# Kernel tuning notes

Hardware: AMD Instinct MI355X
Metric: run time of the kernel (lower is better)

## Reference

```python
import jax, jax.numpy as jnp
import numpy as np

NUM_HEADS = 16

def rotate_half(x):
    h = x.shape[-1] // 2
    return jnp.concatenate([-x[..., h:], x[..., :h]], axis=-1)

def setup_inputs() -> dict:
    key = jax.random.key(0)
    k1, k2, k3 = jax.random.split(key, 3)
    B, S, H = 2, 2048, 1024
    x = jax.random.normal(k1, (B, S, H), dtype=jnp.float32)
    W_qkv = jax.random.normal(k2, (3 * H, H), dtype=jnp.float32) * (1.0 / np.sqrt(H))
    W_proj = jax.random.normal(k3, (H, H), dtype=jnp.float32) * (1.0 / np.sqrt(H))
    return {"x": x, "W_qkv": W_qkv, "W_proj": W_proj}

def reference(x, W_qkv, W_proj):
    B, S, H = x.shape
    nH = NUM_HEADS
    hd = H // nH
    # QKV projection (bias=False): y = x @ W.T
    qkv = jnp.einsum('bsh,oh->bso', x, W_qkv)  # [B,S,3H]
    q, k, v = jnp.split(qkv, 3, axis=-1)
    def to_heads(t):
        return t.reshape(B, S, nH, hd).transpose(0, 2, 1, 3)  # [B,nH,S,hd]
    q, k, v = to_heads(q), to_heads(k), to_heads(v)
    # RoPE on first half of head_dim; freqs dim = hd//2
    half = hd // 2
    inv_freq = 1.0 / (10000.0 ** (jnp.arange(0, hd, 2, dtype=jnp.float32) / hd))  # [hd//2]
    t = jnp.arange(S, dtype=jnp.float32)
    freqs = t[:, None] * inv_freq[None, :]  # [S, hd//2]
    cos = jnp.cos(freqs)[None, None]  # [1,1,S,hd//2]
    sin = jnp.sin(freqs)[None, None]
    q_half, q_rest = q[..., :half], q[..., half:]
    k_half, k_rest = k[..., :half], k[..., half:]
    q_rot = q_half * cos + rotate_half(q_half) * sin
    k_rot = k_half * cos + rotate_half(k_half) * sin
    q = jnp.concatenate([q_rot, q_rest], axis=-1)
    k = jnp.concatenate([k_rot, k_rest], axis=-1)
    # scaled dot-product attention (no mask, dropout=0 / eval)
    scale = 1.0 / np.sqrt(hd)
    att = jnp.einsum('bhqd,bhkd->bhqk', q, k) * scale  # [B,nH,S,S]
    att = jax.nn.softmax(att, axis=-1)
    out = jnp.einsum('bhqk,bhkd->bhqd', att, v)  # [B,nH,S,hd]
    out = out.transpose(0, 2, 1, 3).reshape(B, S, H)
    return jnp.einsum('bsh,oh->bso', out, W_proj)
```

## Files before the change

### kernel.cpp

```cpp
#include <hip/hip_runtime.h>
#include <math.h>

#define SEQ  2048
#define NHD  16
#define HD   64
#define HDIM 1024

typedef short s16x8 __attribute__((ext_vector_type(8)));
typedef short s16x4 __attribute__((ext_vector_type(4)));
typedef float f32x4 __attribute__((ext_vector_type(4)));

typedef const __attribute__((address_space(1))) unsigned int* gp_t;
typedef __attribute__((address_space(3))) unsigned int* lp_t;

__device__ __forceinline__ void async16(const short* g, short* l) {
    __builtin_amdgcn_global_load_lds((gp_t)g, (lp_t)l, 16, 0, 0);
}

__device__ __forceinline__ short f2bf(float f) {
    unsigned int u = __float_as_uint(f);
    u += 0x7fff + ((u >> 16) & 1);
    return (short)(u >> 16);
}
__device__ __forceinline__ float bf2f(short s) {
    return __uint_as_float(((unsigned int)(unsigned short)s) << 16);
}

__global__ void detect_k(const unsigned short* __restrict__ x, int* __restrict__ flag) {
    int cnt = 0;
    #pragma unroll 4
    for (int j = 0; j < 32; ++j) {
        unsigned short h = x[threadIdx.x * 32 + j];
        int e = (h >> 7) & 0xFF;
        cnt += (e >= 100 && e <= 140) ? 1 : 0;
    }
    __shared__ int tot;
    if (threadIdx.x == 0) tot = 0;
    __syncthreads();
    atomicAdd(&tot, cnt);
    __syncthreads();
    if (threadIdx.x == 0) *flag = (tot > (8192 * 9) / 10) ? 1 : 0;
}

#define XG4  (4096 * 1024 / 4)
#define WQG4 (3072 * 1024 / 4)
#define WPG4 (1024 * 1024 / 4)
__global__ void cvt_all_k(const void* __restrict__ xr, const void* __restrict__ wqr,
                          const void* __restrict__ wpr, short* __restrict__ xo,
                          short* __restrict__ wqo, short* __restrict__ wpo,
                          const int* __restrict__ flag) {
    int i = blockIdx.x * 256 + threadIdx.x;
    const void* in; short* out; int j;
    if (i < XG4)             { in = xr;  out = xo;  j = i; }
    else if (i < XG4 + WQG4) { in = wqr; out = wqo; j = i - XG4; }
    else                     { in = wpr; out = wpo; j = i - XG4 - WQG4; }
    if (*flag) {
        ((s16x4*)out)[j] = ((const s16x4*)in)[j];
    } else {
        f32x4 v = ((const f32x4*)in)[j];
        s16x4 r;
        r[0] = f2bf(v[0]); r[1] = f2bf(v[1]);
        r[2] = f2bf(v[2]); r[3] = f2bf(v[3]);
        ((s16x4*)out)[j] = r;
    }
}

__global__ void rope_tab_k(float2* __restrict__ tab) {
    int i = blockIdx.x * 256 + threadIdx.x;
    if (i >= SEQ * 32) return;
    int s = i >> 5, d = i & 31;
    float invf = (float)pow(10000.0, -(double)d / 32.0);
    float af = (float)s * invf;
    double a = (double)af;
    tab[i] = make_float2((float)cos(a), (float)sin(a));
}

template<int MODE>
__global__ __launch_bounds__(256, 2)
void gemm_bt(const short* __restrict__ A, const short* __restrict__ B,
             short* __restrict__ q, short* __restrict__ kbuf, short* __restrict__ vt,
             float* __restrict__ C, const float2* __restrict__ tab,
             int K, int N) {
    __shared__ __align__(16) short As[2][128 * 32];
    __shared__ __align__(16) short Bs[2][128 * 32];
    const int tid  = threadIdx.x;
    const int w    = tid >> 6, lane = tid & 63;
    const int quad = lane >> 4, l16 = lane & 15;
    const int wm = (w >> 1) * 64, wn = (w & 1) * 64;
    const int rowA0 = blockIdx.y * 128;
    const int colB0 = blockIdx.x * 128;

    auto stage = [&](int buf, int kb) {
        #pragma unroll
        for (int i = 0; i < 2; ++i) {
            int cidx = i * 256 + w * 64 + lane;
            int row = cidx >> 2, sc = cidx & 3;
            int c = sc ^ (row & 3);
            async16(&A[(long)(rowA0 + row) * K + kb + c * 8],
                    &As[buf][(i * 256 + w * 64) * 8]);
            async16(&B[(long)(colB0 + row) * K + kb + c * 8],
                    &Bs[buf][(i * 256 + w * 64) * 8]);
        }
    };

    f32x4 acc[4][4] = {};
    stage(0, 0);

    for (int kb = 0, it = 0; kb < K; kb += 32, ++it) {
        const int cur = it & 1;
        __syncthreads();
        if (kb + 32 < K) stage(cur ^ 1, kb + 32);

        s16x8 af[4], bfr[4];
        const int slot = quad ^ (l16 & 3);
        #pragma unroll
        for (int mi = 0; mi < 4; ++mi)
            af[mi] = *(const s16x8*)&As[cur][(wm + mi * 16 + l16) * 32 + slot * 8];
        #pragma unroll
        for (int ni = 0; ni < 4; ++ni)
            bfr[ni] = *(const s16x8*)&Bs[cur][(wn + ni * 16 + l16) * 32 + slot * 8];
        #pragma unroll
        for (int mi = 0; mi < 4; ++mi)
            #pragma unroll
            for (int ni = 0; ni < 4; ++ni)
                acc[mi][ni] = __builtin_amdgcn_mfma_f32_16x16x32_bf16(
                    af[mi], bfr[ni], acc[mi][ni], 0, 0, 0);
    }

    const int cb = colB0 + wn;
    if (MODE == 1) {
        #pragma unroll
        for (int mi = 0; mi < 4; ++mi) {
            #pragma unroll
            for (int r = 0; r < 4; ++r) {
                int gm = rowA0 + wm + mi * 16 + quad * 4 + r;
                float* cp = C + (long)gm * N + cb + l16;
                #pragma unroll
                for (int ni = 0; ni < 4; ++ni)
                    cp[ni * 16] = acc[mi][ni][r];
            }
        }
        return;
    }
    const int sector = cb >> 10;
    const int head   = (cb & 1023) >> 6;
    if (sector < 2) {
        const float sc = (sector == 0) ? 0.18033688f : 1.0f;
        __syncthreads();
        short* arena = (w < 2) ? (&As[0][0] + w * 2048) : (&Bs[0][0] + (w - 2) * 2048);
        const int gmb = rowA0 + wm;
        const int b = gmb >> 11, s0 = gmb & 2047;
        short* dst0 = (sector == 0 ? q : kbuf)
                    + ((long)((b * NHD + head) * SEQ + s0)) * HD;
        #pragma unroll
        for (int hh = 0; hh < 2; ++hh) {
            #pragma unroll
            for (int m2 = 0; m2 < 2; ++m2) {
                int mi = hh * 2 + m2;
                #pragma unroll
                for (int r = 0; r < 4; ++r) {
                    int lrow = m2 * 16 + quad * 4 + r;
                    int s = s0 + hh * 32 + lrow;
                    float v0 = acc[mi][0][r], v1 = acc[mi][1][r];
                    float v2 = acc[mi][2][r], v3 = acc[mi][3][r];
                    float2 cs0 = tab[s * 32 + l16];
                    float2 cs1 = tab[s * 32 + 16 + l16];
                    float n0 = v0 * cs0.x - v1 * cs0.y;
                    float n1 = v1 * cs1.x + v0 * cs1.y;
                    arena[lrow * 64 + l16]      = f2bf(n0 * sc);
                    arena[lrow * 64 + l16 + 16] = f2bf(n1 * sc);
                    arena[lrow * 64 + l16 + 32] = f2bf(v2 * sc);
                    arena[lrow * 64 + l16 + 48] = f2bf(v3 * sc);
                }
            }
            #pragma unroll
            for (int it = 0; it < 4; ++it) {
                int chunk = it * 64 + lane;
                int row = chunk >> 3, cc = chunk & 7;
                s16x8 vv = *(const s16x8*)&arena[row * 64 + cc * 8];
                *(s16x8*)&dst0[(hh * 32 + row) * HD + cc * 8] = vv;
            }
        }
    } else {
        #pragma unroll
        for (int mi = 0; mi < 4; ++mi) {
            int srow = rowA0 + wm + mi * 16 + quad * 4;
            int b = srow >> 11, s0 = srow & 2047;
            #pragma unroll
            for (int ni = 0; ni < 4; ++ni) {
                s16x4 pk;
                #pragma unroll
                for (int r = 0; r < 4; ++r) pk[r] = f2bf(acc[mi][ni][r]);
                *(s16x4*)&vt[((long)((b * NHD + head) * HD + ni * 16 + l16)) * SEQ + s0] = pk;
            }
        }
    }
}

__global__ __launch_bounds__(256, 4)
void flash_attn(const short* __restrict__ Q, const short* __restrict__ K,
                const short* __restrict__ Vt, short* __restrict__ opart,
                float* __restrict__ lpart, int nt) {
    __shared__ __align__(16) short Ks[2][64 * 64];
    __shared__ __align__(16) short Vs[2][64 * 64];
    const int tid  = threadIdx.x;
    const int w    = tid >> 6, lane = tid & 63;
    const int quad = lane >> 4, l16 = lane & 15;
    const int bh = blockIdx.x >> 1;
    const int z  = blockIdx.x & 1;
    const int qb = blockIdx.y * 128;
    const short* Qp = Q  + (long)bh * SEQ * HD + (long)qb * HD;
    const short* Kp = K  + (long)bh * SEQ * HD;
    const short* Vp = Vt + (long)bh * HD * SEQ;
    const int kt0 = z * nt;

    auto stage = [&](int buf, int kt) {
        #pragma unroll
        for (int i = 0; i < 2; ++i) {
            int cidx = i * 256 + w * 64 + lane;
            int row = cidx >> 3, sc = cidx & 7;
            int c = sc ^ (row & 7);
            async16(&Kp[(kt * 64 + row) * HD + c * 8],
                    &Ks[buf][(i * 256 + w * 64) * 8]);
            async16(&Vp[(long)row * SEQ + kt * 64 + c * 8],
                    &Vs[buf][(i * 256 + w * 64) * 8]);
        }
    };

    s16x8 aq[2][2];
    #pragma unroll
    for (int mi = 0; mi < 2; ++mi)
        #pragma unroll
        for (int ks = 0; ks < 2; ++ks)
            aq[mi][ks] = *(const s16x8*)&Qp[(w * 32 + mi * 16 + l16) * HD
                                            + ks * 32 + quad * 8];

    s16x8 ones8;
    #pragma unroll
    for (int j = 0; j < 8; ++j) ones8[j] = (short)0x3F80;

    f32x4 oacc[2][4] = {};
    f32x4 lacc[2] = {};

    stage(0, kt0);
    for (int it = 0; it < nt; ++it) {
        const int cur = it & 1;
        __syncthreads();
        if (it + 1 < nt) stage(cur ^ 1, kt0 + it + 1);

        f32x4 st[2][4] = {};
        #pragma unroll
        for (int ki = 0; ki < 4; ++ki) {
            s16x8 ak0 = *(const s16x8*)&Ks[cur][(ki * 16 + l16) * 64 + (quad ^ (l16 & 7)) * 8];
            s16x8 ak1 = *(const s16x8*)&Ks[cur][(ki * 16 + l16) * 64 + ((4 + quad) ^ (l16 & 7)) * 8];
            #pragma unroll
            for (int mi = 0; mi < 2; ++mi) {
                st[mi][ki] = __builtin_amdgcn_mfma_f32_16x16x32_bf16(
                    ak0, aq[mi][0], st[mi][ki], 0, 0, 0);
                st[mi][ki] = __builtin_amdgcn_mfma_f32_16x16x32_bf16(
                    ak1, aq[mi][1], st[mi][ki], 0, 0, 0);
            }
        }

        s16x8 bp[2][2];
        #pragma unroll
        for (int mi = 0; mi < 2; ++mi)
            #pragma unroll
            for (int t = 0; t < 2; ++t) {
                s16x8 f;
                #pragma unroll
                for (int r = 0; r < 4; ++r) {
                    f[r]     = f2bf(exp2f(st[mi][2 * t][r]));
                    f[4 + r] = f2bf(exp2f(st[mi][2 * t + 1][r]));
                }
                bp[mi][t] = f;
            }

        #pragma unroll
        for (int t = 0; t < 2; ++t) {
            #pragma unroll
            for (int nd = 0; nd < 4; ++nd) {
                int d = nd * 16 + l16;
                s16x4 va = *(const s16x4*)&Vs[cur][d * 64
                             + ((4 * t + (quad >> 1)) ^ (l16 & 7)) * 8
                             + (quad & 1) * 4];
                s16x4 vb = *(const s16x4*)&Vs[cur][d * 64
                             + ((4 * t + 2 + (quad >> 1)) ^ (l16 & 7)) * 8
                             + (quad & 1) * 4];
                s16x8 av = {va[0], va[1], va[2], va[3],
                            vb[0], vb[1], vb[2], vb[3]};
                #pragma unroll
                for (int mi = 0; mi < 2; ++mi)
                    oacc[mi][nd] = __builtin_amdgcn_mfma_f32_16x16x32_bf16(
                        av, bp[mi][t], oacc[mi][nd], 0, 0, 0);
            }
            #pragma unroll
            for (int mi = 0; mi < 2; ++mi)
                lacc[mi] = __builtin_amdgcn_mfma_f32_16x16x32_bf16(
                    ones8, bp[mi][t], lacc[mi], 0, 0, 0);
        }
    }

    #pragma unroll
    for (int mi = 0; mi < 2; ++mi) {
        int srow = qb + w * 32 + mi * 16 + l16;
        long prow = (long)(z * 2 * NHD + bh) * SEQ + srow;
        if (quad == 0) lpart[prow] = lacc[mi][0];
        short* op = opart + prow * 64 + quad * 4;
        #pragma unroll
        for (int nd = 0; nd < 4; ++nd) {
            s16x4 pk;
            #pragma unroll
            for (int r = 0; r < 4; ++r) pk[r] = f2bf(oacc[mi][nd][r]);
            *(s16x4*)&op[nd * 16] = pk;
        }
    }
}

__global__ __launch_bounds__(256)
void merge_k(const short* __restrict__ opart, const float* __restrict__ lpart,
             short* __restrict__ att) {
    int idx = blockIdx.x * 256 + threadIdx.x;
    int t16 = idx & 15, rowg = idx >> 4;
    int bh = rowg >> 11, srow = rowg & 2047;
    float inv = 1.0f / (lpart[rowg] + lpart[65536 + rowg]);
    s16x4 o1 = *(const s16x4*)&opart[(long)rowg * 64 + t16 * 4];
    s16x4 o2 = *(const s16x4*)&opart[(long)(65536 + rowg) * 64 + t16 * 4];
    int b = bh >> 4, h = bh & 15;
    short* dst = att + ((long)(b * SEQ + srow)) * HDIM + h * HD + t16 * 4;
    s16x4 r;
    #pragma unroll
    for (int j = 0; j < 4; ++j)
        r[j] = f2bf((bf2f(o1[j]) + bf2f(o2[j])) * inv);
    *(s16x4*)dst = r;
}

extern "C" void kernel_launch(void* const* d_in, const int* in_sizes, int n_in,
                              void* d_out, int out_size, void* d_ws, size_t ws_size,
                              hipStream_t stream) {
    const void* x_raw  = d_in[0];
    const void* Wq_raw = d_in[1];
    const void* Wp_raw = d_in[2];
    for (int i = 0; i < n_in; ++i) {
        if      (in_sizes[i] == 4096 * 1024) x_raw  = d_in[i];
        else if (in_sizes[i] == 3072 * 1024) Wq_raw = d_in[i];
        else if (in_sizes[i] == 1024 * 1024) Wp_raw = d_in[i];
    }
    float* out = (float*)d_out;

    const size_t MB = 1u << 20;
    char* ws = (char*)d_ws;
    short*  q     = (short*)(ws);
    short*  k     = (short*)(ws +  8 * MB);
    short*  vt    = (short*)(ws + 16 * MB);
    short*  xbf   = (short*)(ws + 24 * MB);
    short*  att   = xbf;
    short*  wqkv  = (short*)(ws + 32 * MB);
    short*  wprj  = (short*)(ws + 38 * MB);
    float2* tab   = (float2*)(ws + 40 * MB);
    int*    flag  = (int*)(ws + 40 * MB + 512 * 1024);
    short*  opart = (short*)(ws + 41 * MB);
    float*  lprt  = (float*)(ws + 57 * MB);

    detect_k<<<dim3(1), dim3(256), 0, stream>>>((const unsigned short*)x_raw, flag);

    cvt_all_k<<<dim3((XG4 + WQG4 + WPG4) / 256), dim3(256), 0, stream>>>(
        x_raw, Wq_raw, Wp_raw, xbf, wqkv, wprj, flag);

    rope_tab_k<<<dim3(SEQ * 32 / 256), dim3(256), 0, stream>>>(tab);

    gemm_bt<0><<<dim3(3072 / 128, 4096 / 128), dim3(256), 0, stream>>>(
        xbf, wqkv, q, k, vt, (float*)nullptr, tab, 1024, 3072);

    flash_attn<<<dim3(2 * NHD * 2, SEQ / 128), dim3(256), 0, stream>>>(
        q, k, vt, opart, lprt, 16);

    merge_k<<<dim3(65536 * 16 / 256), dim3(256), 0, stream>>>(opart, lprt, att);

    gemm_bt<1><<<dim3(1024 / 128, 4096 / 128), dim3(256), 0, stream>>>(
        att, wprj, (short*)nullptr, (short*)nullptr, (short*)nullptr, out, tab, 1024, 1024);
}
```

Before: 209.7 us.

## Stage V-transpose epilogue through swizzled LDS and pack bf16 with perm

The QKV GEMM epilogue now stages the full 64x64 tile per wave through an XOR-swizzled LDS arena. This lets both the Q/K path and the transposed V path write 16-byte coalesced rows to global memory, where the V path previously did scattered 8-byte stores with a 2048-element stride. Separately, float-to-bf16 conversions in the convert, softmax-P, output-partial and merge kernels use a round-half-up add plus a byte-permute packing two values per instruction, instead of round-to-nearest-even per element. The arena doubles to 4096 shorts per wave, and the rounding change slightly alters numerics on ties.

Measured after the change: 205.3 us. 1.02x faster.

```diff
diff --git a/kernel.cpp b/kernel.cpp
--- a/kernel.cpp
+++ b/kernel.cpp
@@ -24,6 +24,11 @@
 }
 __device__ __forceinline__ float bf2f(short s) {
     return __uint_as_float(((unsigned int)(unsigned short)s) << 16);
+}
+__device__ __forceinline__ unsigned pkbf(float a, float b) {
+    unsigned ua = __float_as_uint(a) + 0x8000u;
+    unsigned ub = __float_as_uint(b) + 0x8000u;
+    return __builtin_amdgcn_perm(ua, ub, 0x03020706u);
 }
 
 __global__ void detect_k(const unsigned short* __restrict__ x, int* __restrict__ flag) {
@@ -58,10 +63,10 @@
         ((s16x4*)out)[j] = ((const s16x4*)in)[j];
     } else {
         f32x4 v = ((const f32x4*)in)[j];
-        s16x4 r;
-        r[0] = f2bf(v[0]); r[1] = f2bf(v[1]);
-        r[2] = f2bf(v[2]); r[3] = f2bf(v[3]);
-        ((s16x4*)out)[j] = r;
+        union { unsigned u[2]; s16x4 v; } r;
+        r.u[0] = pkbf(v[0], v[1]);
+        r.u[1] = pkbf(v[2], v[3]);
+        ((s16x4*)out)[j] = r.v;
     }
 }
 
@@ -144,55 +149,59 @@
     }
     const int sector = cb >> 10;
     const int head   = (cb & 1023) >> 6;
+    const int gmb = rowA0 + wm;
+    const int b = gmb >> 11, s0 = gmb & 2047;
+    __syncthreads();
+    short* arena = (w < 2) ? (&As[0][0] + w * 4096) : (&Bs[0][0] + (w - 2) * 4096);
+    auto aw = [&](int row, int col, short val) {
+        arena[row * 64 + (((col >> 3) ^ (row & 7)) << 3) + (col & 7)] = val;
+    };
     if (sector < 2) {
         const float sc = (sector == 0) ? 0.18033688f : 1.0f;
-        __syncthreads();
-        short* arena = (w < 2) ? (&As[0][0] + w * 2048) : (&Bs[0][0] + (w - 2) * 2048);
-        const int gmb = rowA0 + wm;
-        const int b = gmb >> 11, s0 = gmb & 2047;
+        #pragma unroll
+        for (int mi = 0; mi < 4; ++mi) {
+            #pragma unroll
+            for (int r = 0; r < 4; ++r) {
+                int lrow = mi * 16 + quad * 4 + r;
+                int s = s0 + lrow;
+                float v0 = acc[mi][0][r], v1 = acc[mi][1][r];
+                float v2 = acc[mi][2][r], v3 = acc[mi][3][r];
+                float2 cs0 = tab[s * 32 + l16];
+                float2 cs1 = tab[s * 32 + 16 + l16];
+                float n0 = v0 * cs0.x - v1 * cs0.y;
+                float n1 = v1 * cs1.x + v0 * cs1.y;
+                aw(lrow, l16,      f2bf(n0 * sc));
+                aw(lrow, l16 + 16, f2bf(n1 * sc));
+                aw(lrow, l16 + 32, f2bf(v2 * sc));
+                aw(lrow, l16 + 48, f2bf(v3 * sc));
+            }
+        }
         short* dst0 = (sector == 0 ? q : kbuf)
                     + ((long)((b * NHD + head) * SEQ + s0)) * HD;
         #pragma unroll
-        for (int hh = 0; hh < 2; ++hh) {
-            #pragma unroll
-            for (int m2 = 0; m2 < 2; ++m2) {
-                int mi = hh * 2 + m2;
-                #pragma unroll
-                for (int r = 0; r < 4; ++r) {
-                    int lrow = m2 * 16 + quad * 4 + r;
-                    int s = s0 + hh * 32 + lrow;
-                    float v0 = acc[mi][0][r], v1 = acc[mi][1][r];
-                    float v2 = acc[mi][2][r], v3 = acc[mi][3][r];
-                    float2 cs0 = tab[s * 32 + l16];
-                    float2 cs1 = tab[s * 32 + 16 + l16];
-                    float n0 = v0 * cs0.x - v1 * cs0.y;
-                    float n1 = v1 * cs1.x + v0 * cs1.y;
-                    arena[lrow * 64 + l16]      = f2bf(n0 * sc);
-                    arena[lrow * 64 + l16 + 16] = f2bf(n1 * sc);
-                    arena[lrow * 64 + l16 + 32] = f2bf(v2 * sc);
-                    arena[lrow * 64 + l16 + 48] = f2bf(v3 * sc);
-                }
-            }
-            #pragma unroll
-            for (int it = 0; it < 4; ++it) {
-                int chunk = it * 64 + lane;
-                int row = chunk >> 3, cc = chunk & 7;
-                s16x8 vv = *(const s16x8*)&arena[row * 64 + cc * 8];
-                *(s16x8*)&dst0[(hh * 32 + row) * HD + cc * 8] = vv;
-            }
+        for (int it = 0; it < 8; ++it) {
+            int row = it * 8 + (lane >> 3), cc = lane & 7;
+            s16x8 vv = *(const s16x8*)&arena[row * 64 + ((cc ^ (row & 7)) << 3)];
+            *(s16x8*)&dst0[row * HD + cc * 8] = vv;
         }
     } else {
         #pragma unroll
         for (int mi = 0; mi < 4; ++mi) {
-            int srow = rowA0 + wm + mi * 16 + quad * 4;
-            int b = srow >> 11, s0 = srow & 2047;
-            #pragma unroll
-            for (int ni = 0; ni < 4; ++ni) {
-                s16x4 pk;
-                #pragma unroll
-                for (int r = 0; r < 4; ++r) pk[r] = f2bf(acc[mi][ni][r]);
-                *(s16x4*)&vt[((long)((b * NHD + head) * HD + ni * 16 + l16)) * SEQ + s0] = pk;
-            }
+            #pragma unroll
+            for (int r = 0; r < 4; ++r) {
+                int scol = mi * 16 + quad * 4 + r;
+                aw(l16,      scol, f2bf(acc[mi][0][r]));
+                aw(l16 + 16, scol, f2bf(acc[mi][1][r]));
+                aw(l16 + 32, scol, f2bf(acc[mi][2][r]));
+                aw(l16 + 48, scol, f2bf(acc[mi][3][r]));
+            }
+        }
+        short* dstv = vt + ((long)((b * NHD + head) * HD)) * SEQ + s0;
+        #pragma unroll
+        for (int it = 0; it < 8; ++it) {
+            int dd = it * 8 + (lane >> 3), so8 = lane & 7;
+            s16x8 vv = *(const s16x8*)&arena[dd * 64 + ((so8 ^ (dd & 7)) << 3)];
+            *(s16x8*)&dstv[(long)dd * SEQ + so8 * 8] = vv;
         }
     }
 }
@@ -267,13 +276,12 @@
         for (int mi = 0; mi < 2; ++mi)
             #pragma unroll
             for (int t = 0; t < 2; ++t) {
-                s16x8 f;
-                #pragma unroll
-                for (int r = 0; r < 4; ++r) {
-                    f[r]     = f2bf(exp2f(st[mi][2 * t][r]));
-                    f[4 + r] = f2bf(exp2f(st[mi][2 * t + 1][r]));
-                }
-                bp[mi][t] = f;
+                union { unsigned u[4]; s16x8 v; } pk;
+                pk.u[0] = pkbf(exp2f(st[mi][2 * t][0]),     exp2f(st[mi][2 * t][1]));
+                pk.u[1] = pkbf(exp2f(st[mi][2 * t][2]),     exp2f(st[mi][2 * t][3]));
+                pk.u[2] = pkbf(exp2f(st[mi][2 * t + 1][0]), exp2f(st[mi][2 * t + 1][1]));
+                pk.u[3] = pkbf(exp2f(st[mi][2 * t + 1][2]), exp2f(st[mi][2 * t + 1][3]));
+                bp[mi][t] = pk.v;
             }
 
         #pragma unroll
@@ -309,10 +317,10 @@
         short* op = opart + prow * 64 + quad * 4;
         #pragma unroll
         for (int nd = 0; nd < 4; ++nd) {
-            s16x4 pk;
-            #pragma unroll
-            for (int r = 0; r < 4; ++r) pk[r] = f2bf(oacc[mi][nd][r]);
-            *(s16x4*)&op[nd * 16] = pk;
+            union { unsigned u[2]; s16x4 v; } pk;
+            pk.u[0] = pkbf(oacc[mi][nd][0], oacc[mi][nd][1]);
+            pk.u[1] = pkbf(oacc[mi][nd][2], oacc[mi][nd][3]);
+            *(s16x4*)&op[nd * 16] = pk.v;
         }
     }
 }
@@ -328,11 +336,12 @@
     s16x4 o2 = *(const s16x4*)&opart[(long)(65536 + rowg) * 64 + t16 * 4];
     int b = bh >> 4, h = bh & 15;
     short* dst = att + ((long)(b * SEQ + srow)) * HDIM + h * HD + t16 * 4;
-    s16x4 r;
-    #pragma unroll
-    for (int j = 0; j < 4; ++j)
-        r[j] = f2bf((bf2f(o1[j]) + bf2f(o2[j])) * inv);
-    *(s16x4*)dst = r;
+    union { unsigned u[2]; s16x4 v; } r;
+    r.u[0] = pkbf((bf2f(o1[0]) + bf2f(o2[0])) * inv,
+                  (bf2f(o1[1]) + bf2f(o2[1])) * inv);
+    r.u[1] = pkbf((bf2f(o1[2]) + bf2f(o2[2])) * inv,
+                  (bf2f(o1[3]) + bf2f(o2[3])) * inv);
+    *(s16x4*)dst = r.v;
 }
 
 extern "C" void kernel_launch(void* const* d_in, const int* in_sizes, int n_in,
```
